# Performance work log

Measured on AMD Instinct MI355X. Metric: run time of the kernel, lower is better.

Reference implementation:

```python
import jax, jax.numpy as jnp
import numpy as np

B, S, DM, H = 8, 1024, 1024, 16
D = DM // H  # head dim = 64


def setup_inputs() -> dict:
    key = jax.random.key(0)
    ks = jax.random.split(key, 10)
    Q = jax.random.normal(ks[0], (B, S, DM), jnp.float32)
    K = jax.random.normal(ks[1], (B, S, DM), jnp.float32)
    V = jax.random.normal(ks[2], (B, S, DM), jnp.float32)
    pad = jax.random.randint(ks[3], (B,), 0, 512)
    sc = 0.02
    Wq = jax.random.normal(ks[4], (H, DM, D), jnp.float32) * sc
    Wk = jax.random.normal(ks[5], (H, DM, D), jnp.float32) * sc
    Wv = jax.random.normal(ks[6], (H, DM, D), jnp.float32) * sc
    bq = jnp.zeros((H, D), jnp.float32)
    bk = jnp.zeros((H, D), jnp.float32)
    bv = jnp.zeros((H, D), jnp.float32)
    Wo = jax.random.normal(ks[7], (DM, DM), jnp.float32) * sc
    bo = jnp.zeros((DM,), jnp.float32)
    return {"Q": Q, "K": K, "V": V, "pad": pad,
            "Wq": Wq, "bq": bq, "Wk": Wk, "bk": bk,
            "Wv": Wv, "bv": bv, "Wo": Wo, "bo": bo}


def reference(Q, K, V, pad, Wq, bq, Wk, bk, Wv, bv, Wo, bo):
    seq = Q.shape[1]
    # per-head projections, batched over heads: [B,H,S,D]
    Qh = jnp.einsum('bsm,hmd->bhsd', Q, Wq) + bq[None, :, None, :]
    Kh = jnp.einsum('bsm,hmd->bhsd', K, Wk) + bk[None, :, None, :]
    Vh = jnp.einsum('bsm,hmd->bhsd', V, Wv) + bv[None, :, None, :]
    # NOTE: original divides by sqrt(seq_len) (K.shape[1]), not sqrt(head_dim)
    scores = jnp.einsum('bhsd,bhtd->bhst', Qh, Kh) / jnp.sqrt(jnp.float32(seq))
    t = jnp.arange(seq)
    # padding mask over keys: last pad[b] positions; pad==0 masks ALL (torch -0: quirk)
    pad_mask = (t[None, :] >= seq - pad[:, None]) | (pad[:, None] == 0)  # [B,T]
    causal = t[None, :] > t[:, None]  # [S,T], strict upper triangle
    M = jnp.maximum(pad_mask[:, None, None, :].astype(jnp.float32),
                    causal[None, None, :, :].astype(jnp.float32))
    scores = scores + M * (-1e9)
    att = jax.nn.softmax(scores, axis=-1)
    Xh = jnp.einsum('bhst,bhtd->bhsd', att, Vh)
    # concat heads along last dim (head order preserved)
    X = Xh.transpose(0, 2, 1, 3).reshape(Q.shape[0], seq, H * D)
    return X @ Wo + bo
```

## Files before the change

kernel.cpp:

```cpp
#include <hip/hip_runtime.h>
#include <cmath>

#define BATCH 8
#define SEQ 1024
#define DMODEL 1024
#define NHEAD 16
#define HDIM 64
#define USE_GLOAD 1

typedef _Float16 f16x8 __attribute__((ext_vector_type(8)));
typedef _Float16 f16x4 __attribute__((ext_vector_type(4)));
typedef _Float16 f16x2 __attribute__((ext_vector_type(2)));
typedef float    f32x4 __attribute__((ext_vector_type(4)));


__global__ __launch_bounds__(256)
void prep_cvt(const float* __restrict__ Q, const float* __restrict__ K,
              const float* __restrict__ V, _Float16* __restrict__ Qf,
              _Float16* __restrict__ Kf, _Float16* __restrict__ Vf)
{
    const int n = (8192 * 1024) / 4;
    const float*   src = (blockIdx.y == 0) ? Q : (blockIdx.y == 1) ? K : V;
    _Float16*      dst = (blockIdx.y == 0) ? Qf : (blockIdx.y == 1) ? Kf : Vf;
    for (int i = blockIdx.x * 256 + threadIdx.x; i < n; i += gridDim.x * 256) {
        const float4 v = ((const float4*)src)[i];
        ((f16x4*)dst)[i] = (f16x4){ (_Float16)v.x, (_Float16)v.y,
                                    (_Float16)v.z, (_Float16)v.w };
    }
}

__global__ __launch_bounds__(256)
void prep_tr(const float* __restrict__ Wq, const float* __restrict__ Wk,
             const float* __restrict__ Wv, const float* __restrict__ Wo,
             _Float16* __restrict__ WqT, _Float16* __restrict__ WkT,
             _Float16* __restrict__ WvT, _Float16* __restrict__ WoT)
{
    __shared__ float L[64][65];
    const int z  = blockIdx.z;
    const int t  = threadIdx.x;
    const float*    W  = (z == 0) ? Wq : (z == 1) ? Wk : (z == 2) ? Wv : Wo;
    _Float16*       WT = (z == 0) ? WqT : (z == 1) ? WkT : (z == 2) ? WvT : WoT;
    const int k0 = blockIdx.y * 64;
    const int n0 = blockIdx.x * 64;
    const int kr = t >> 2, c4 = (t & 3) * 16;
    const float* src = (z < 3)
        ? &W[((size_t)blockIdx.x * DMODEL + (k0 + kr)) * HDIM + c4]
        : &W[(size_t)(k0 + kr) * DMODEL + n0 + c4];
    #pragma unroll
    for (int j = 0; j < 4; ++j) {
        const float4 v = *(const float4*)(src + j * 4);
        L[kr][c4 + j * 4 + 0] = v.x; L[kr][c4 + j * 4 + 1] = v.y;
        L[kr][c4 + j * 4 + 2] = v.z; L[kr][c4 + j * 4 + 3] = v.w;
    }
    __syncthreads();
    const int d = t >> 2, kk = (t & 3) * 16;
    f16x8 o0, o1;
    #pragma unroll
    for (int j = 0; j < 8; ++j) {
        o0[j] = (_Float16)L[kk + j][d];
        o1[j] = (_Float16)L[kk + 8 + j][d];
    }
    *(f16x8*)&WT[(size_t)(n0 + d) * DMODEL + k0 + kk]     = o0;
    *(f16x8*)&WT[(size_t)(n0 + d) * DMODEL + k0 + kk + 8] = o1;
}

template<int OLAYOUT>
__global__ __launch_bounds__(256)
void gemm_f16(const _Float16* __restrict__ A, const _Float16* __restrict__ BT,
              const float* __restrict__ bias, float* __restrict__ Cf,
              _Float16* __restrict__ Ch)
{
    constexpr int Kd = DMODEL;
    alignas(16) __shared__ _Float16 Al[128 * 64];
    alignas(16) __shared__ _Float16 Bl[128 * 64];

    const int t    = threadIdx.x;
    const int lane = t & 63;
    const int w    = t >> 6;
    const int wr   = w >> 1, wc = w & 1;
    const int q    = lane >> 4, r = lane & 15;
    const int m0   = blockIdx.y * 128;
    const int n0   = blockIdx.x * 128;
    const int srow = lane >> 3;
    const int sslot = lane & 7;

    f32x4 acc[4][4];
    #pragma unroll
    for (int i = 0; i < 4; ++i)
        #pragma unroll
        for (int j = 0; j < 4; ++j)
            acc[i][j] = (f32x4){0.f, 0.f, 0.f, 0.f};

    for (int kt = 0; kt < Kd / 64; ++kt) {
        const int k0 = kt * 64;
        #pragma unroll
        for (int j = 0; j < 4; ++j) {
            const int rowA = w * 32 + j * 8 + srow;
            const int colA = ((sslot ^ (rowA & 7)) << 3);
#if USE_GLOAD
            __builtin_amdgcn_global_load_lds(
                (const __attribute__((address_space(1))) void*)
                    &A[(size_t)(m0 + rowA) * Kd + k0 + colA],
                (__attribute__((address_space(3))) void*)&Al[(w * 32 + j * 8) * 64],
                16, 0, 0);
#else
            *(f16x8*)&Al[(size_t)rowA * 64 + (sslot << 3)] =
                *(const f16x8*)&A[(size_t)(m0 + rowA) * Kd + k0 + colA];
#endif
        }
        #pragma unroll
        for (int j = 0; j < 4; ++j) {
            const int rowB = w * 32 + j * 8 + srow;
            const int colB = ((sslot ^ (rowB & 7)) << 3);
#if USE_GLOAD
            __builtin_amdgcn_global_load_lds(
                (const __attribute__((address_space(1))) void*)
                    &BT[(size_t)(n0 + rowB) * Kd + k0 + colB],
                (__attribute__((address_space(3))) void*)&Bl[(w * 32 + j * 8) * 64],
                16, 0, 0);
#else
            *(f16x8*)&Bl[(size_t)rowB * 64 + (sslot << 3)] =
                *(const f16x8*)&BT[(size_t)(n0 + rowB) * Kd + k0 + colB];
#endif
        }
        __syncthreads();
        #pragma unroll
        for (int h = 0; h < 2; ++h) {
            f16x8 a[4], b[4];
            #pragma unroll
            for (int mf = 0; mf < 4; ++mf) {
                const int row = wr * 64 + mf * 16 + r;
                a[mf] = *(const f16x8*)&Al[row * 64 + (((h * 4 + q) ^ (row & 7)) << 3)];
            }
            #pragma unroll
            for (int nf = 0; nf < 4; ++nf) {
                const int row = wc * 64 + nf * 16 + r;
                b[nf] = *(const f16x8*)&Bl[row * 64 + (((h * 4 + q) ^ (row & 7)) << 3)];
            }
            #pragma unroll
            for (int mf = 0; mf < 4; ++mf)
                #pragma unroll
                for (int nf = 0; nf < 4; ++nf)
                    acc[mf][nf] = __builtin_amdgcn_mfma_f32_16x16x32_f16(
                        a[mf], b[nf], acc[mf][nf], 0, 0, 0);
        }
        __syncthreads();
    }

    #pragma unroll
    for (int mf = 0; mf < 4; ++mf) {
        #pragma unroll
        for (int nf = 0; nf < 4; ++nf) {
            const int col = n0 + wc * 64 + nf * 16 + r;
            const float bv = bias[col];
            #pragma unroll
            for (int i = 0; i < 4; ++i) {
                const int row = m0 + wr * 64 + mf * 16 + q * 4 + i;
                const float val = acc[mf][nf][i] + bv;
                if (OLAYOUT == 0) {
                    const int bb = row >> 10, s = row & 1023;
                    const int h = col >> 6, d = col & 63;
                    Ch[((((size_t)bb * NHEAD + h) << 10) + s) * HDIM + d] = (_Float16)val;
                } else {
                    Cf[(size_t)row * DMODEL + col] = val;
                }
            }
        }
    }
}

__global__ __launch_bounds__(512, 4)
void attn_mfma(const _Float16* __restrict__ Qh, const _Float16* __restrict__ Kh,
               const _Float16* __restrict__ Vh, const int* __restrict__ pad,
               _Float16* __restrict__ X)
{
    alignas(16) __shared__ _Float16 Klds[64 * 64];
    alignas(16) __shared__ _Float16 VT[64][72];
    alignas(16) __shared__ _Float16 Plds[8][16][72];

    const int tid  = threadIdx.x;
    const int w    = tid >> 6;
    const int lane = tid & 63;
    const int qq   = lane >> 4;
    const int r    = lane & 15;
    const int bh   = blockIdx.y;
    const int b    = bh >> 4;
    const int hh   = bh & 15;
    const int s0   = blockIdx.x << 7;
    const int padb = pad[b];
    const size_t base = (size_t)bh * SEQ * HDIM;
    const int mrow = s0 + w * 16;

    f16x8 qf[2];
    #pragma unroll
    for (int kh = 0; kh < 2; ++kh)
        qf[kh] = *(const f16x8*)&Qh[base + (size_t)(mrow + r) * HDIM + kh * 32 + qq * 8];

    const int kvlim = (padb == 0) ? SEQ : (SEQ - padb);
    const int Lblk  = (padb == 0) ? SEQ : min(s0 + 128, SEQ - padb);
    const int nt    = (Lblk + 63) >> 6;

    float mrun[4], lrun[4];
    f32x4 accO[4];
    #pragma unroll
    for (int i = 0; i < 4; ++i) {
        mrun[i] = -3.0e38f; lrun[i] = 0.f;
        accO[i] = (f32x4){0.f, 0.f, 0.f, 0.f};
    }

    const int krow  = w * 8 + (lane >> 3);
    const int kslot = lane & 7;
    const int tp = tid >> 4, dq = tid & 15;

    for (int kt = 0; kt < nt; ++kt) {
        const int t0 = kt << 6;
        __syncthreads();
#if USE_GLOAD
        __builtin_amdgcn_global_load_lds(
            (const __attribute__((address_space(1))) void*)
                &Kh[base + (size_t)(t0 + krow) * HDIM + ((kslot ^ (krow & 7)) << 3)],
            (__attribute__((address_space(3))) void*)&Klds[w * 8 * 64],
            16, 0, 0);
#else
        *(f16x8*)&Klds[krow * 64 + (kslot << 3)] =
            *(const f16x8*)&Kh[base + (size_t)(t0 + krow) * HDIM + ((kslot ^ (krow & 7)) << 3)];
#endif
        {
            const f16x4 a0 = *(const f16x4*)&Vh[base + (size_t)(t0 + 2 * tp) * HDIM + 4 * dq];
            const f16x4 a1 = *(const f16x4*)&Vh[base + (size_t)(t0 + 2 * tp + 1) * HDIM + 4 * dq];
            #pragma unroll
            for (int c = 0; c < 4; ++c)
                *(f16x2*)&VT[4 * dq + c][2 * tp] = (f16x2){ a0[c], a1[c] };
        }
        __syncthreads();

        f32x4 sacc[4];
        #pragma unroll
        for (int tg = 0; tg < 4; ++tg) sacc[tg] = (f32x4){0.f, 0.f, 0.f, 0.f};
        #pragma unroll
        for (int tg = 0; tg < 4; ++tg)
            #pragma unroll
            for (int kh = 0; kh < 2; ++kh) {
                const int kr = tg * 16 + r;
                const f16x8 kf = *(const f16x8*)
                    &Klds[kr * 64 + (((kh * 4 + qq) ^ (kr & 7)) << 3)];
                sacc[tg] = __builtin_amdgcn_mfma_f32_16x16x32_f16(qf[kh], kf, sacc[tg], 0, 0, 0);
            }

        float sc[4][4];
        #pragma unroll
        for (int tg = 0; tg < 4; ++tg) {
            const int tt = t0 + tg * 16 + r;
            #pragma unroll
            for (int i = 0; i < 4; ++i) {
                const int mm = mrow + qq * 4 + i;
                float x = sacc[tg][i] * 0.03125f;
                if (tt > mm || tt >= kvlim || padb == 0)
                    x -= 1.0e9f;
                sc[tg][i] = x;
            }
        }
        float p[4][4], scale[4];
        #pragma unroll
        for (int i = 0; i < 4; ++i) {
            float mx = fmaxf(fmaxf(sc[0][i], sc[1][i]), fmaxf(sc[2][i], sc[3][i]));
            #pragma unroll
            for (int off = 1; off < 16; off <<= 1)
                mx = fmaxf(mx, __shfl_xor(mx, off));
            const float mn = fmaxf(mrun[i], mx);
            scale[i] = __expf(mrun[i] - mn);
            mrun[i] = mn;
            float ls = 0.f;
            #pragma unroll
            for (int tg = 0; tg < 4; ++tg) {
                const float pv = __expf(sc[tg][i] - mn);
                p[tg][i] = pv;
                ls += pv;
            }
            #pragma unroll
            for (int off = 1; off < 16; off <<= 1)
                ls += __shfl_xor(ls, off);
            lrun[i] = lrun[i] * scale[i] + ls;
        }

        #pragma unroll
        for (int tg = 0; tg < 4; ++tg)
            #pragma unroll
            for (int i = 0; i < 4; ++i)
                Plds[w][qq * 4 + i][tg * 16 + r] = (_Float16)p[tg][i];
        asm volatile("s_waitcnt lgkmcnt(0)" ::: "memory");
        __builtin_amdgcn_wave_barrier();

        const f16x8 pa0 = *(const f16x8*)&Plds[w][r][qq * 8];
        const f16x8 pa1 = *(const f16x8*)&Plds[w][r][32 + qq * 8];

        #pragma unroll
        for (int dg = 0; dg < 4; ++dg) {
            #pragma unroll
            for (int i = 0; i < 4; ++i) accO[dg][i] *= scale[i];
            const f16x8 v0f = *(const f16x8*)&VT[dg * 16 + r][qq * 8];
            const f16x8 v1f = *(const f16x8*)&VT[dg * 16 + r][32 + qq * 8];
            accO[dg] = __builtin_amdgcn_mfma_f32_16x16x32_f16(pa0, v0f, accO[dg], 0, 0, 0);
            accO[dg] = __builtin_amdgcn_mfma_f32_16x16x32_f16(pa1, v1f, accO[dg], 0, 0, 0);
        }
    }

    #pragma unroll
    for (int dg = 0; dg < 4; ++dg)
        #pragma unroll
        for (int i = 0; i < 4; ++i)
            X[((size_t)b * SEQ + (mrow + qq * 4 + i)) * DMODEL + hh * HDIM + dg * 16 + r] =
                (_Float16)(accO[dg][i] / lrun[i]);
}

extern "C" void kernel_launch(void* const* d_in, const int* in_sizes, int n_in,
                              void* d_out, int out_size, void* d_ws, size_t ws_size,
                              hipStream_t stream)
{
    const float* Q  = (const float*)d_in[0];
    const float* K  = (const float*)d_in[1];
    const float* V  = (const float*)d_in[2];
    const int*  pad = (const int*)d_in[3];
    const float* Wq = (const float*)d_in[4];
    const float* bq = (const float*)d_in[5];
    const float* Wk = (const float*)d_in[6];
    const float* bk = (const float*)d_in[7];
    const float* Wv = (const float*)d_in[8];
    const float* bv = (const float*)d_in[9];
    const float* Wo = (const float*)d_in[10];
    const float* bo = (const float*)d_in[11];
    float* out = (float*)d_out;

    char* ws = (char*)d_ws;
    const size_t MB = 1024 * 1024;
    _Float16* Qf16 = (_Float16*)(ws + 0 * MB);
    _Float16* Kf16 = (_Float16*)(ws + 16 * MB);
    _Float16* Vf16 = (_Float16*)(ws + 32 * MB);
    _Float16* WqT  = (_Float16*)(ws + 48 * MB);
    _Float16* WkT  = (_Float16*)(ws + 50 * MB);
    _Float16* WvT  = (_Float16*)(ws + 52 * MB);
    _Float16* WoT  = (_Float16*)(ws + 54 * MB);
    _Float16* Qh   = (_Float16*)(ws + 56 * MB);
    _Float16* Kh   = (_Float16*)(ws + 72 * MB);
    _Float16* Vh   = (_Float16*)(ws + 0 * MB);
    _Float16* X    = (_Float16*)(ws + 16 * MB);

    prep_cvt<<<dim3(1024, 3), 256, 0, stream>>>(Q, K, V, Qf16, Kf16, Vf16);
    prep_tr <<<dim3(16, 16, 4), 256, 0, stream>>>(Wq, Wk, Wv, Wo, WqT, WkT, WvT, WoT);

    dim3 gg(DMODEL / 128, (BATCH * SEQ) / 128);
    gemm_f16<0><<<gg, 256, 0, stream>>>(Qf16, WqT, bq, nullptr, Qh);
    gemm_f16<0><<<gg, 256, 0, stream>>>(Kf16, WkT, bk, nullptr, Kh);
    gemm_f16<0><<<gg, 256, 0, stream>>>(Vf16, WvT, bv, nullptr, Vh);

    attn_mfma<<<dim3(SEQ / 128, BATCH * NHEAD), 512, 0, stream>>>(Qh, Kh, Vh, pad, X);

    gemm_f16<1><<<gg, 256, 0, stream>>>(X, WoT, bo, out, nullptr);
}
```

Measured before the change: 371.5 us.

## Pre-transpose V globally and use 64-row attention blocks with async LDS loads

Adds a separate kernel that transposes the V head tensor into a [d][seq] layout, so the attention kernel can load V tiles straight into LDS with global_load_lds and XOR swizzling instead of scattering transposed stores. The attention block drops from 128 query rows and 512 threads to 64 rows and 256 threads, doubling the grid and reducing how many KV tiles of padded work each block covers. The P scratch buffer is also swizzled to avoid bank conflicts. The cost is an extra kernel launch and an extra round trip of V through global memory, plus K/V tiles being reloaded by twice as many blocks.

```diff
diff --git a/kernel.cpp b/kernel.cpp
--- a/kernel.cpp
+++ b/kernel.cpp
@@ -64,6 +64,32 @@
     *(f16x8*)&WT[(size_t)(n0 + d) * DMODEL + k0 + kk + 8] = o1;
 }
 
+__global__ __launch_bounds__(256)
+void transpose_v(const _Float16* __restrict__ Vh, _Float16* __restrict__ VT)
+{
+    __shared__ _Float16 L[64][72];
+    const int bh = blockIdx.y;
+    const int s0 = blockIdx.x * 64;
+    const int t  = threadIdx.x;
+    const size_t base = (size_t)bh * SEQ * HDIM;
+    {
+        const _Float16* src = &Vh[base + (size_t)(s0 + (t >> 2)) * HDIM + (t & 3) * 16];
+        *(f16x8*)&L[t >> 2][(t & 3) * 16]     = *(const f16x8*)src;
+        *(f16x8*)&L[t >> 2][(t & 3) * 16 + 8] = *(const f16x8*)(src + 8);
+    }
+    __syncthreads();
+    const int d = t >> 2, sq = (t & 3) * 16;
+    f16x8 o0, o1;
+    #pragma unroll
+    for (int j = 0; j < 8; ++j) {
+        o0[j] = L[sq + j][d];
+        o1[j] = L[sq + 8 + j][d];
+    }
+    _Float16* dst = &VT[base + (size_t)d * SEQ + s0 + sq];
+    *(f16x8*)dst       = o0;
+    *(f16x8*)(dst + 8) = o1;
+}
+
 template<int OLAYOUT>
 __global__ __launch_bounds__(256)
 void gemm_f16(const _Float16* __restrict__ A, const _Float16* __restrict__ BT,
@@ -97,31 +123,21 @@
         for (int j = 0; j < 4; ++j) {
             const int rowA = w * 32 + j * 8 + srow;
             const int colA = ((sslot ^ (rowA & 7)) << 3);
-#if USE_GLOAD
             __builtin_amdgcn_global_load_lds(
                 (const __attribute__((address_space(1))) void*)
                     &A[(size_t)(m0 + rowA) * Kd + k0 + colA],
                 (__attribute__((address_space(3))) void*)&Al[(w * 32 + j * 8) * 64],
                 16, 0, 0);
-#else
-            *(f16x8*)&Al[(size_t)rowA * 64 + (sslot << 3)] =
-                *(const f16x8*)&A[(size_t)(m0 + rowA) * Kd + k0 + colA];
-#endif
         }
         #pragma unroll
         for (int j = 0; j < 4; ++j) {
             const int rowB = w * 32 + j * 8 + srow;
             const int colB = ((sslot ^ (rowB & 7)) << 3);
-#if USE_GLOAD
             __builtin_amdgcn_global_load_lds(
                 (const __attribute__((address_space(1))) void*)
                     &BT[(size_t)(n0 + rowB) * Kd + k0 + colB],
                 (__attribute__((address_space(3))) void*)&Bl[(w * 32 + j * 8) * 64],
                 16, 0, 0);
-#else
-            *(f16x8*)&Bl[(size_t)rowB * 64 + (sslot << 3)] =
-                *(const f16x8*)&BT[(size_t)(n0 + rowB) * Kd + k0 + colB];
-#endif
         }
         __syncthreads();
         #pragma unroll
@@ -169,14 +185,14 @@
     }
 }
 
-__global__ __launch_bounds__(512, 4)
+__global__ __launch_bounds__(256)
 void attn_mfma(const _Float16* __restrict__ Qh, const _Float16* __restrict__ Kh,
-               const _Float16* __restrict__ Vh, const int* __restrict__ pad,
+               const _Float16* __restrict__ VT, const int* __restrict__ pad,
                _Float16* __restrict__ X)
 {
     alignas(16) __shared__ _Float16 Klds[64 * 64];
-    alignas(16) __shared__ _Float16 VT[64][72];
-    alignas(16) __shared__ _Float16 Plds[8][16][72];
+    alignas(16) __shared__ _Float16 Vlds[64 * 64];
+    alignas(16) __shared__ _Float16 Plds[4][16 * 64];
 
     const int tid  = threadIdx.x;
     const int w    = tid >> 6;
@@ -186,7 +202,7 @@
     const int bh   = blockIdx.y;
     const int b    = bh >> 4;
     const int hh   = bh & 15;
-    const int s0   = blockIdx.x << 7;
+    const int s0   = blockIdx.x << 6;
     const int padb = pad[b];
     const size_t base = (size_t)bh * SEQ * HDIM;
     const int mrow = s0 + w * 16;
@@ -197,7 +213,7 @@
         qf[kh] = *(const f16x8*)&Qh[base + (size_t)(mrow + r) * HDIM + kh * 32 + qq * 8];
 
     const int kvlim = (padb == 0) ? SEQ : (SEQ - padb);
-    const int Lblk  = (padb == 0) ? SEQ : min(s0 + 128, SEQ - padb);
+    const int Lblk  = (padb == 0) ? SEQ : min(s0 + 64, SEQ - padb);
     const int nt    = (Lblk + 63) >> 6;
 
     float mrun[4], lrun[4];
@@ -208,29 +224,31 @@
         accO[i] = (f32x4){0.f, 0.f, 0.f, 0.f};
     }
 
-    const int krow  = w * 8 + (lane >> 3);
-    const int kslot = lane & 7;
-    const int tp = tid >> 4, dq = tid & 15;
+    const int srow  = lane >> 3;
+    const int sslot = lane & 7;
 
     for (int kt = 0; kt < nt; ++kt) {
         const int t0 = kt << 6;
         __syncthreads();
-#if USE_GLOAD
-        __builtin_amdgcn_global_load_lds(
-            (const __attribute__((address_space(1))) void*)
-                &Kh[base + (size_t)(t0 + krow) * HDIM + ((kslot ^ (krow & 7)) << 3)],
-            (__attribute__((address_space(3))) void*)&Klds[w * 8 * 64],
-            16, 0, 0);
-#else
-        *(f16x8*)&Klds[krow * 64 + (kslot << 3)] =
-            *(const f16x8*)&Kh[base + (size_t)(t0 + krow) * HDIM + ((kslot ^ (krow & 7)) << 3)];
-#endif
-        {
-            const f16x4 a0 = *(const f16x4*)&Vh[base + (size_t)(t0 + 2 * tp) * HDIM + 4 * dq];
-            const f16x4 a1 = *(const f16x4*)&Vh[base + (size_t)(t0 + 2 * tp + 1) * HDIM + 4 * dq];
-            #pragma unroll
-            for (int c = 0; c < 4; ++c)
-                *(f16x2*)&VT[4 * dq + c][2 * tp] = (f16x2){ a0[c], a1[c] };
+        #pragma unroll
+        for (int j = 0; j < 2; ++j) {
+            const int row = j * 32 + w * 8 + srow;
+            const int col = ((sslot ^ (row & 7)) << 3);
+            __builtin_amdgcn_global_load_lds(
+                (const __attribute__((address_space(1))) void*)
+                    &Kh[base + (size_t)(t0 + row) * HDIM + col],
+                (__attribute__((address_space(3))) void*)&Klds[(j * 32 + w * 8) * 64],
+                16, 0, 0);
+        }
+        #pragma unroll
+        for (int j = 0; j < 2; ++j) {
+            const int row = j * 32 + w * 8 + srow;
+            const int col = ((sslot ^ (row & 7)) << 3);
+            __builtin_amdgcn_global_load_lds(
+                (const __attribute__((address_space(1))) void*)
+                    &VT[base + (size_t)row * SEQ + t0 + col],
+                (__attribute__((address_space(3))) void*)&Vlds[(j * 32 + w * 8) * 64],
+                16, 0, 0);
         }
         __syncthreads();
 
@@ -286,22 +304,32 @@
         #pragma unroll
         for (int tg = 0; tg < 4; ++tg)
             #pragma unroll
-            for (int i = 0; i < 4; ++i)
-                Plds[w][qq * 4 + i][tg * 16 + r] = (_Float16)p[tg][i];
+            for (int i = 0; i < 4; ++i) {
+                const int m  = qq * 4 + i;
+                const int tt = tg * 16 + r;
+                Plds[w][m * 64 + (((tt >> 3) ^ (m & 7)) << 3) + (tt & 7)] =
+                    (_Float16)p[tg][i];
+            }
         asm volatile("s_waitcnt lgkmcnt(0)" ::: "memory");
         __builtin_amdgcn_wave_barrier();
 
-        const f16x8 pa0 = *(const f16x8*)&Plds[w][r][qq * 8];
-        const f16x8 pa1 = *(const f16x8*)&Plds[w][r][32 + qq * 8];
+        f16x8 pa[2];
+        #pragma unroll
+        for (int kh = 0; kh < 2; ++kh)
+            pa[kh] = *(const f16x8*)
+                &Plds[w][r * 64 + (((kh * 4 + qq) ^ (r & 7)) << 3)];
 
         #pragma unroll
         for (int dg = 0; dg < 4; ++dg) {
             #pragma unroll
             for (int i = 0; i < 4; ++i) accO[dg][i] *= scale[i];
-            const f16x8 v0f = *(const f16x8*)&VT[dg * 16 + r][qq * 8];
-            const f16x8 v1f = *(const f16x8*)&VT[dg * 16 + r][32 + qq * 8];
-            accO[dg] = __builtin_amdgcn_mfma_f32_16x16x32_f16(pa0, v0f, accO[dg], 0, 0, 0);
-            accO[dg] = __builtin_amdgcn_mfma_f32_16x16x32_f16(pa1, v1f, accO[dg], 0, 0, 0);
+            #pragma unroll
+            for (int kh = 0; kh < 2; ++kh) {
+                const int vrow = dg * 16 + r;
+                const f16x8 vf = *(const f16x8*)
+                    &Vlds[vrow * 64 + (((kh * 4 + qq) ^ (vrow & 7)) << 3)];
+                accO[dg] = __builtin_amdgcn_mfma_f32_16x16x32_f16(pa[kh], vf, accO[dg], 0, 0, 0);
+            }
         }
     }
 
@@ -343,7 +371,8 @@
     _Float16* Qh   = (_Float16*)(ws + 56 * MB);
     _Float16* Kh   = (_Float16*)(ws + 72 * MB);
     _Float16* Vh   = (_Float16*)(ws + 0 * MB);
-    _Float16* X    = (_Float16*)(ws + 16 * MB);
+    _Float16* VT   = (_Float16*)(ws + 16 * MB);
+    _Float16* X    = (_Float16*)(ws + 32 * MB);
 
     prep_cvt<<<dim3(1024, 3), 256, 0, stream>>>(Q, K, V, Qf16, Kf16, Vf16);
     prep_tr <<<dim3(16, 16, 4), 256, 0, stream>>>(Wq, Wk, Wv, Wo, WqT, WkT, WvT, WoT);
@@ -353,7 +382,9 @@
     gemm_f16<0><<<gg, 256, 0, stream>>>(Kf16, WkT, bk, nullptr, Kh);
     gemm_f16<0><<<gg, 256, 0, stream>>>(Vf16, WvT, bv, nullptr, Vh);
 
-    attn_mfma<<<dim3(SEQ / 128, BATCH * NHEAD), 512, 0, stream>>>(Qh, Kh, Vh, pad, X);
+    transpose_v<<<dim3(SEQ / 64, BATCH * NHEAD), 256, 0, stream>>>(Vh, VT);
+
+    attn_mfma<<<dim3(SEQ / 64, BATCH * NHEAD), 256, 0, stream>>>(Qh, Kh, VT, pad, X);
 
     gemm_f16<1><<<gg, 256, 0, stream>>>(X, WoT, bo, out, nullptr);
 }
```

Result: no change. 371.4 us (-0.0%).
